# Kernel optimization log

Measured on AMD Instinct MI355X. Metric: run time of the kernel, lower is better.

Reference implementation:

```python
import jax, jax.numpy as jnp
import numpy as np

B, T, C = 2, 4096, 1024
H = 16            # n_head (== n_groups == n_kv_heads)
HD = C // H       # head_dim = 64
W = 256           # window_size
ROPE_BASE = 10000.0


def _rope(x):
    # x: (B, H, T, HD); rotate interleaved pairs with position along axis 2
    t = x.shape[2]
    inv_freq = 1.0 / (ROPE_BASE ** (jnp.arange(0, HD, 2, dtype=jnp.float32) / HD))  # (HD/2,)
    freqs = jnp.arange(t, dtype=jnp.float32)[:, None] * inv_freq[None, :]           # (T, HD/2)
    cos = jnp.cos(freqs)[None, None].astype(x.dtype)
    sin = jnp.sin(freqs)[None, None].astype(x.dtype)
    x1, x2 = x[..., 0::2], x[..., 1::2]
    o1 = x1 * cos - x2 * sin
    o2 = x1 * sin + x2 * cos
    return jnp.stack([o1, o2], axis=-1).reshape(x.shape)


def setup_inputs() -> dict:
    key = jax.random.key(0)
    ks = jax.random.split(key, 5)
    s = 1.0 / np.sqrt(C)
    return {
        "x": jax.random.normal(ks[0], (B, T, C), dtype=jnp.float32),
        "wq": jax.random.normal(ks[1], (C, C), dtype=jnp.float32) * s,
        "wk": jax.random.normal(ks[2], (C, C), dtype=jnp.float32) * s,
        "wv": jax.random.normal(ks[3], (C, C), dtype=jnp.float32) * s,
        "wo": jax.random.normal(ks[4], (C, C), dtype=jnp.float32) * s,
    }


def reference(x, wq, wk, wv, wo):
    # projections (Linear stores (out, in) -> x @ w.T)
    q = jnp.einsum('btc,oc->bto', x, wq).reshape(B, T, H, HD).transpose(0, 2, 1, 3)
    k = jnp.einsum('btc,oc->bto', x, wk).reshape(B, T, H, HD).transpose(0, 2, 1, 3)
    v = jnp.einsum('btc,oc->bto', x, wv).reshape(B, T, H, HD).transpose(0, 2, 1, 3)

    q = _rope(q)
    k = _rope(k)

    nW = T // W
    qw = q.reshape(B, H, nW, W, HD)
    kw = k.reshape(B, H, nW, W, HD)
    vw = v.reshape(B, H, nW, W, HD)

    scale = 1.0 / jnp.sqrt(jnp.asarray(HD, dtype=q.dtype))
    att = jnp.einsum('bhnqd,bhnkd->bhnqk', qw, kw) * scale   # per-window, no causal mask
    att = jax.nn.softmax(att, axis=-1)
    yw = jnp.einsum('bhnqk,bhnkd->bhnqd', att, vw)

    y = yw.reshape(B, H, T, HD).transpose(0, 2, 1, 3).reshape(B, T, C)
    return jnp.einsum('btc,oc->bto', y, wo)
```

## Files before the change

kernel.cpp:

```cpp
#include <hip/hip_runtime.h>
#include <math.h>

typedef float f32x4 __attribute__((ext_vector_type(4)));
typedef __bf16 bf16x8 __attribute__((ext_vector_type(8)));
typedef unsigned short u16x8 __attribute__((ext_vector_type(8)));
typedef unsigned short ushort_t;

#define MFMA16(a, b, c) __builtin_amdgcn_mfma_f32_16x16x32_bf16((a), (b), (c), 0, 0, 0)

static __device__ __forceinline__ ushort_t f2bf(float f) {
  union { float f; unsigned u; } v; v.f = f;
  unsigned u = v.u;
  return (ushort_t)((u + 0x7FFFu + ((u >> 16) & 1u)) >> 16);
}
static __device__ __forceinline__ float bf2f(ushort_t h) {
  union { unsigned u; float f; } v; v.u = ((unsigned)h) << 16;
  return v.f;
}
static __device__ __forceinline__ void gl_lds16(const void* g, void* lds_uniform) {
  __builtin_amdgcn_global_load_lds(
      (const __attribute__((address_space(1))) unsigned int*)g,
      (__attribute__((address_space(3))) unsigned int*)lds_uniform, 16, 0, 0);
}

__global__ void prep(const float* __restrict__ x,
                     const float* __restrict__ wq, const float* __restrict__ wk,
                     const float* __restrict__ wv, const float* __restrict__ wo,
                     ushort_t* __restrict__ Xb, ushort_t* __restrict__ Wqb,
                     ushort_t* __restrict__ Wkb, ushort_t* __restrict__ Wvb,
                     ushort_t* __restrict__ Wob, float2* __restrict__ cs) {
  const int bid = blockIdx.x;
  if (bid < 512) {
    int idx = bid * 256 + threadIdx.x;
    int pos = idx >> 5, i = idx & 31;
    double inv = exp2(-(double)i * 0.41524101186092029);
    double th = (double)pos * inv;
    double s, c;
    sincos(th, &s, &c);
    cs[idx] = make_float2((float)c, (float)s);
  } else {
    const float* src;
    ushort_t* dst;
    int i;
    if (bid < 8704) {
      src = x; dst = Xb;
      i = (bid - 512) * 256 + threadIdx.x;
    } else {
      const int wi = (bid - 8704) >> 10;
      src = (wi == 0) ? wq : (wi == 1) ? wk : (wi == 2) ? wv : wo;
      dst = (wi == 0) ? Wqb : (wi == 1) ? Wkb : (wi == 2) ? Wvb : Wob;
      i = ((bid - 8704) & 1023) * 256 + threadIdx.x;
    }
    f32x4 v = ((const f32x4*)src)[i];
    ushort4 o;
    o.x = f2bf(v.x); o.y = f2bf(v.y); o.z = f2bf(v.z); o.w = f2bf(v.w);
    ((ushort4*)dst)[i] = o;
  }
}

template <int OUTBF>
__global__ __launch_bounds__(256) void gemm_nt(
    const ushort_t* __restrict__ A,
    const ushort_t* __restrict__ W0, const ushort_t* __restrict__ W1, const ushort_t* __restrict__ W2,
    void* __restrict__ C0, void* __restrict__ C1, void* __restrict__ C2,
    int K, int N) {
  __shared__ __align__(16) ushort_t As[128 * 64];
  __shared__ __align__(16) ushort_t Bs[128 * 64];
  const int z = blockIdx.z;
  const ushort_t* W = (z == 0) ? W0 : (z == 1 ? W1 : W2);
  void* Cv = (z == 0) ? C0 : (z == 1 ? C1 : C2);

  const int t = threadIdx.x;
  const int lane = t & 63;
  const int l15 = lane & 15;
  const int quad = lane >> 4;
  const int wave = t >> 6;
  const int wm = wave & 1, wn = wave >> 1;
  const int bm = blockIdx.x, bn = blockIdx.y;

  const int srow = t >> 3;
  const int schunk = (t & 7) ^ (srow & 7);
  const ushort_t* Ag = A + (size_t)(bm * 128 + srow) * K + schunk * 8;
  const ushort_t* Wg = W + (size_t)(bn * 128 + srow) * K + schunk * 8;
  char* AsB = (char*)As + (t & 192) * 16;
  char* BsB = (char*)Bs + (t & 192) * 16;
  const size_t rK = (size_t)32 * K;

  const f32x4 zero4 = {0.f, 0.f, 0.f, 0.f};
  f32x4 acc[4][4];
#pragma unroll
  for (int i = 0; i < 4; ++i)
#pragma unroll
    for (int j = 0; j < 4; ++j) acc[i][j] = zero4;

  for (int kt = 0; kt < K; kt += 64) {
#pragma unroll
    for (int p = 0; p < 4; ++p) {
      gl_lds16(Ag + p * rK + kt, AsB + p * 4096);
      gl_lds16(Wg + p * rK + kt, BsB + p * 4096);
    }
    __syncthreads();
#pragma unroll
    for (int ks = 0; ks < 2; ++ks) {
      bf16x8 af[4], bfr[4];
#pragma unroll
      for (int i = 0; i < 4; ++i) {
        const int r = wm * 64 + i * 16 + l15;
        af[i] = *(const bf16x8*)&As[r * 64 + (((ks * 4 + quad) ^ (r & 7)) * 8)];
      }
#pragma unroll
      for (int j = 0; j < 4; ++j) {
        const int r = wn * 64 + j * 16 + l15;
        bfr[j] = *(const bf16x8*)&Bs[r * 64 + (((ks * 4 + quad) ^ (r & 7)) * 8)];
      }
#pragma unroll
      for (int i = 0; i < 4; ++i)
#pragma unroll
        for (int j = 0; j < 4; ++j) acc[i][j] = MFMA16(af[i], bfr[j], acc[i][j]);
    }
    __syncthreads();
  }

  const int rbase = bm * 128 + wm * 64 + quad * 4;
  const int cbase = bn * 128 + wn * 64 + l15;
#pragma unroll
  for (int i = 0; i < 4; ++i)
#pragma unroll
    for (int j = 0; j < 4; ++j)
#pragma unroll
      for (int r = 0; r < 4; ++r) {
        size_t idx = (size_t)(rbase + i * 16 + r) * N + (cbase + j * 16);
        if (OUTBF)
          ((ushort_t*)Cv)[idx] = f2bf(acc[i][j][r]);
        else
          ((float*)Cv)[idx] = acc[i][j][r];
      }
}

static __device__ __forceinline__ void rope8(const ushort_t* __restrict__ g,
                                             ushort_t* __restrict__ lds,
                                             const float2* __restrict__ cs4) {
  uint4 raw = *(const uint4*)g;
  unsigned rw[4] = {raw.x, raw.y, raw.z, raw.w};
  ushort_t o[8];
#pragma unroll
  for (int m = 0; m < 4; ++m) {
    float x1 = bf2f((ushort_t)(rw[m] & 0xffffu));
    float x2 = bf2f((ushort_t)(rw[m] >> 16));
    float2 sc = cs4[m];
    o[2 * m]     = f2bf(x1 * sc.x - x2 * sc.y);
    o[2 * m + 1] = f2bf(x1 * sc.y + x2 * sc.x);
  }
  uint4 w;
  w.x = (unsigned)o[0] | ((unsigned)o[1] << 16);
  w.y = (unsigned)o[2] | ((unsigned)o[3] << 16);
  w.z = (unsigned)o[4] | ((unsigned)o[5] << 16);
  w.w = (unsigned)o[6] | ((unsigned)o[7] << 16);
  *(uint4*)lds = w;
}

__global__ __launch_bounds__(256) void attn(
    const ushort_t* __restrict__ Qb, const ushort_t* __restrict__ Kb,
    const ushort_t* __restrict__ Vb, ushort_t* __restrict__ Yb,
    const float2* __restrict__ cs) {
  __shared__ __align__(16) ushort_t smem[21504];
  ushort_t* Ks = smem;
  ushort_t* Vt = smem;
  ushort_t* Pc = smem + 16896;

  const int t = threadIdx.x;
  const int lane = t & 63, wave = t >> 6;
  const int l15 = lane & 15, quad = lane >> 4;
  const int win = blockIdx.x >> 2, qq = blockIdx.x & 3;
  const int h = blockIdx.y, b = blockIdx.z;
  const int kBase = win * 256;
  const int qRow0 = kBase + qq * 64 + wave * 16;
  const size_t gbase = ((size_t)b * 4096) * 1024 + h * 64;

  const int sr = t >> 3;
  const int c0 = (t & 7) * 8;

#pragma unroll
  for (int p = 0; p < 8; ++p) {
    int r = p * 32 + sr;
    rope8(Kb + gbase + (size_t)(kBase + r) * 1024 + c0, Ks + r * 72 + c0,
          cs + (kBase + r) * 32 + (c0 >> 1));
  }
  __syncthreads();

  const f32x4 zero4 = {0.f, 0.f, 0.f, 0.f};
  f32x4 S[16];
#pragma unroll
  for (int j = 0; j < 16; ++j) S[j] = zero4;
#pragma unroll
  for (int ks = 0; ks < 2; ++ks) {
    union { u16x8 u; bf16x8 b; } aq;
    aq.u = *(const u16x8*)(Qb + gbase + (size_t)(qRow0 + l15) * 1024 + ks * 32 + quad * 8);
    const float2* csq = cs + (size_t)(qRow0 + l15) * 32 + ks * 16 + quad * 4;
#pragma unroll
    for (int m = 0; m < 4; ++m) {
      float x1 = bf2f(aq.u[2 * m]);
      float x2 = bf2f(aq.u[2 * m + 1]);
      float2 sc = csq[m];
      aq.u[2 * m]     = f2bf((x1 * sc.x - x2 * sc.y) * 0.125f);
      aq.u[2 * m + 1] = f2bf((x1 * sc.y + x2 * sc.x) * 0.125f);
    }
#pragma unroll
    for (int j = 0; j < 16; ++j) {
      bf16x8 bk = *(const bf16x8*)&Ks[(j * 16 + l15) * 72 + ks * 32 + quad * 8];
      S[j] = MFMA16(aq.b, bk, S[j]);
    }
  }

  float linv[4];
#pragma unroll
  for (int r = 0; r < 4; ++r) {
    float mx = S[0][r];
#pragma unroll
    for (int j = 1; j < 16; ++j) mx = fmaxf(mx, S[j][r]);
    mx = fmaxf(mx, __shfl_xor(mx, 1));
    mx = fmaxf(mx, __shfl_xor(mx, 2));
    mx = fmaxf(mx, __shfl_xor(mx, 4));
    mx = fmaxf(mx, __shfl_xor(mx, 8));
    float sum = 0.f;
#pragma unroll
    for (int j = 0; j < 16; ++j) {
      float e = __expf(S[j][r] - mx);
      S[j][r] = e;
      sum += e;
    }
    sum += __shfl_xor(sum, 1);
    sum += __shfl_xor(sum, 2);
    sum += __shfl_xor(sum, 4);
    sum += __shfl_xor(sum, 8);
    linv[r] = 1.0f / sum;
  }
  __syncthreads();

#pragma unroll
  for (int p = 0; p < 8; ++p) {
    int k = p * 32 + sr;
    uint4 raw = *(const uint4*)(Vb + gbase + (size_t)(kBase + k) * 1024 + c0);
    ushort_t vv[8];
    vv[0] = raw.x & 0xffffu; vv[1] = raw.x >> 16;
    vv[2] = raw.y & 0xffffu; vv[3] = raw.y >> 16;
    vv[4] = raw.z & 0xffffu; vv[5] = raw.z >> 16;
    vv[6] = raw.w & 0xffffu; vv[7] = raw.w >> 16;
#pragma unroll
    for (int e = 0; e < 8; ++e) {
      int ee = (e + (t & 7)) & 7;
      Vt[(c0 + ee) * 264 + k] = vv[ee];
    }
  }
  __syncthreads();

  const int qw = wave * 16;
  f32x4 O[4];
#pragma unroll
  for (int jd = 0; jd < 4; ++jd) O[jd] = zero4;

#pragma unroll
  for (int kc = 0; kc < 4; ++kc) {
#pragma unroll
    for (int jj = 0; jj < 4; ++jj) {
      int j = kc * 4 + jj;
#pragma unroll
      for (int r = 0; r < 4; ++r)
        Pc[(qw + quad * 4 + r) * 72 + jj * 16 + l15] = f2bf(S[j][r]);
    }
#pragma unroll
    for (int ks = 0; ks < 2; ++ks) {
      bf16x8 a = *(const bf16x8*)&Pc[(qw + l15) * 72 + ks * 32 + quad * 8];
#pragma unroll
      for (int jd = 0; jd < 4; ++jd) {
        bf16x8 bv = *(const bf16x8*)&Vt[(jd * 16 + l15) * 264 + kc * 64 + ks * 32 + quad * 8];
        O[jd] = MFMA16(a, bv, O[jd]);
      }
    }
  }

#pragma unroll
  for (int jd = 0; jd < 4; ++jd)
#pragma unroll
    for (int r = 0; r < 4; ++r) {
      int row = qRow0 + quad * 4 + r;
      Yb[gbase + (size_t)row * 1024 + jd * 16 + l15] = f2bf(O[jd][r] * linv[r]);
    }
}

extern "C" void kernel_launch(void* const* d_in, const int* in_sizes, int n_in,
                              void* d_out, int out_size, void* d_ws, size_t ws_size,
                              hipStream_t stream) {
  (void)in_sizes; (void)n_in; (void)out_size; (void)ws_size;
  const float* x  = (const float*)d_in[0];
  const float* wq = (const float*)d_in[1];
  const float* wk = (const float*)d_in[2];
  const float* wv = (const float*)d_in[3];
  const float* wo = (const float*)d_in[4];

  char* ws = (char*)d_ws;
  ushort_t* Xb  = (ushort_t*)(ws);
  ushort_t* Wqb = (ushort_t*)(ws + 16777216);
  ushort_t* Wkb = Wqb + 1048576;
  ushort_t* Wvb = Wkb + 1048576;
  ushort_t* Wob = Wvb + 1048576;
  ushort_t* Qb  = (ushort_t*)(ws + 25165824);
  ushort_t* Kb  = Qb + 8388608;
  ushort_t* Vb  = Kb + 8388608;
  ushort_t* Yb  = Vb + 8388608;
  float2*   cs  = (float2*)(ws + 92274688);

  prep<<<dim3(12800), dim3(256), 0, stream>>>(x, wq, wk, wv, wo,
                                              Xb, Wqb, Wkb, Wvb, Wob, cs);

  gemm_nt<1><<<dim3(64, 8, 3), dim3(256), 0, stream>>>(
      Xb, Wqb, Wkb, Wvb, (void*)Qb, (void*)Kb, (void*)Vb, 1024, 1024);

  attn<<<dim3(64, 16, 2), dim3(256), 0, stream>>>(Qb, Kb, Vb, Yb, cs);

  gemm_nt<0><<<dim3(64, 8, 1), dim3(256), 0, stream>>>(
      Yb, Wob, Wob, Wob, d_out, d_out, d_out, 1024, 1024);
}
```

Measured before the change: 248.1 us.

## Split RoPE into separate pass and restructure attention with transposed S and fp16 PV

Moves RoPE for Q and K out of the attention kernel into a standalone in-place pass, so attention can load K straight into swizzled LDS with async global_load_lds. It computes S transposed (K as the A operand) so each lane owns one query column, which removes the P round-trip through LDS and lets P feed an fp16 16x16x16 MFMA directly from registers. V is written as fp16 by the QKV GEMM, its loads are hoisted before the barrier, and the output is staged through LDS for coalesced 16-byte stores. This adds one extra kernel launch and a full read/write pass over Q and K, and changes V and P precision to fp16.

```diff
diff --git a/kernel.cpp b/kernel.cpp
--- a/kernel.cpp
+++ b/kernel.cpp
@@ -3,10 +3,11 @@
 
 typedef float f32x4 __attribute__((ext_vector_type(4)));
 typedef __bf16 bf16x8 __attribute__((ext_vector_type(8)));
-typedef unsigned short u16x8 __attribute__((ext_vector_type(8)));
+typedef _Float16 f16x4 __attribute__((ext_vector_type(4)));
 typedef unsigned short ushort_t;
 
 #define MFMA16(a, b, c) __builtin_amdgcn_mfma_f32_16x16x32_bf16((a), (b), (c), 0, 0, 0)
+#define MFMAPV(a, b, c) __builtin_amdgcn_mfma_f32_16x16x16f16((a), (b), (c), 0, 0, 0)
 
 static __device__ __forceinline__ ushort_t f2bf(float f) {
   union { float f; unsigned u; } v; v.f = f;
@@ -58,7 +59,7 @@
   }
 }
 
-template <int OUTBF>
+template <int MODE>
 __global__ __launch_bounds__(256) void gemm_nt(
     const ushort_t* __restrict__ A,
     const ushort_t* __restrict__ W0, const ushort_t* __restrict__ W1, const ushort_t* __restrict__ W2,
@@ -130,49 +131,67 @@
 #pragma unroll
       for (int r = 0; r < 4; ++r) {
         size_t idx = (size_t)(rbase + i * 16 + r) * N + (cbase + j * 16);
-        if (OUTBF)
+        if (MODE == 0) {
+          ((float*)Cv)[idx] = acc[i][j][r];
+        } else if (z == 2) {
+          union { _Float16 h; ushort_t u; } cv;
+          cv.h = (_Float16)acc[i][j][r];
+          ((ushort_t*)Cv)[idx] = cv.u;
+        } else {
           ((ushort_t*)Cv)[idx] = f2bf(acc[i][j][r]);
-        else
-          ((float*)Cv)[idx] = acc[i][j][r];
+        }
       }
 }
 
-static __device__ __forceinline__ void rope8(const ushort_t* __restrict__ g,
-                                             ushort_t* __restrict__ lds,
-                                             const float2* __restrict__ cs4) {
-  uint4 raw = *(const uint4*)g;
+static __device__ __forceinline__ uint4 rope_u4(uint4 raw, const float2* __restrict__ c4,
+                                                float scale) {
   unsigned rw[4] = {raw.x, raw.y, raw.z, raw.w};
   ushort_t o[8];
 #pragma unroll
   for (int m = 0; m < 4; ++m) {
     float x1 = bf2f((ushort_t)(rw[m] & 0xffffu));
     float x2 = bf2f((ushort_t)(rw[m] >> 16));
-    float2 sc = cs4[m];
-    o[2 * m]     = f2bf(x1 * sc.x - x2 * sc.y);
-    o[2 * m + 1] = f2bf(x1 * sc.y + x2 * sc.x);
+    float2 sc = c4[m];
+    o[2 * m]     = f2bf((x1 * sc.x - x2 * sc.y) * scale);
+    o[2 * m + 1] = f2bf((x1 * sc.y + x2 * sc.x) * scale);
   }
   uint4 w;
   w.x = (unsigned)o[0] | ((unsigned)o[1] << 16);
   w.y = (unsigned)o[2] | ((unsigned)o[3] << 16);
   w.z = (unsigned)o[4] | ((unsigned)o[5] << 16);
   w.w = (unsigned)o[6] | ((unsigned)o[7] << 16);
-  *(uint4*)lds = w;
+  return w;
+}
+
+__global__ void ropeqk(ushort_t* __restrict__ Qb, ushort_t* __restrict__ Kb,
+                       const float2* __restrict__ cs) {
+  const int idx0 = blockIdx.x * 256 + threadIdx.x;
+#pragma unroll
+  for (int g = 0; g < 2; ++g) {
+    const int idx = idx0 + g * 524288;
+    const int row = idx >> 7;
+    const int col8 = (idx & 127) << 3;
+    const float2* c4 = cs + (((size_t)(row & 4095)) << 5) + ((col8 & 63) >> 1);
+    uint4 q = ((const uint4*)Qb)[idx];
+    uint4 k = ((const uint4*)Kb)[idx];
+    ((uint4*)Qb)[idx] = rope_u4(q, c4, 0.125f);
+    ((uint4*)Kb)[idx] = rope_u4(k, c4, 1.0f);
+  }
 }
 
 __global__ __launch_bounds__(256) void attn(
     const ushort_t* __restrict__ Qb, const ushort_t* __restrict__ Kb,
-    const ushort_t* __restrict__ Vb, ushort_t* __restrict__ Yb,
-    const float2* __restrict__ cs) {
-  __shared__ __align__(16) ushort_t smem[21504];
+    const ushort_t* __restrict__ Vb, ushort_t* __restrict__ Yb) {
+  __shared__ __align__(16) ushort_t smem[16896];
   ushort_t* Ks = smem;
   ushort_t* Vt = smem;
-  ushort_t* Pc = smem + 16896;
 
   const int t = threadIdx.x;
   const int lane = t & 63, wave = t >> 6;
   const int l15 = lane & 15, quad = lane >> 4;
-  const int win = blockIdx.x >> 2, qq = blockIdx.x & 3;
-  const int h = blockIdx.y, b = blockIdx.z;
+  const int qq = blockIdx.x >> 9;
+  const int s = blockIdx.x & 511;
+  const int win = s & 15, h = (s >> 4) & 15, b = s >> 8;
   const int kBase = win * 256;
   const int qRow0 = kBase + qq * 64 + wave * 16;
   const size_t gbase = ((size_t)b * 4096) * 1024 + h * 64;
@@ -180,12 +199,17 @@
   const int sr = t >> 3;
   const int c0 = (t & 7) * 8;
 
-#pragma unroll
-  for (int p = 0; p < 8; ++p) {
-    int r = p * 32 + sr;
-    rope8(Kb + gbase + (size_t)(kBase + r) * 1024 + c0, Ks + r * 72 + c0,
-          cs + (kBase + r) * 32 + (c0 >> 1));
-  }
+  const int schunk = ((t & 7) ^ (sr & 7)) * 8;
+  const ushort_t* Kg = Kb + gbase + (size_t)(kBase + sr) * 1024 + schunk;
+  char* LdsB = (char*)smem + (t & 192) * 16;
+#pragma unroll
+  for (int p = 0; p < 8; ++p) gl_lds16(Kg + (size_t)p * 32 * 1024, LdsB + p * 4096);
+
+  bf16x8 qf[2];
+#pragma unroll
+  for (int ks = 0; ks < 2; ++ks)
+    qf[ks] = *(const bf16x8*)(Qb + gbase + (size_t)(qRow0 + l15) * 1024 + ks * 32 + quad * 8);
+
   __syncthreads();
 
   const f32x4 zero4 = {0.f, 0.f, 0.f, 0.f};
@@ -193,99 +217,84 @@
 #pragma unroll
   for (int j = 0; j < 16; ++j) S[j] = zero4;
 #pragma unroll
-  for (int ks = 0; ks < 2; ++ks) {
-    union { u16x8 u; bf16x8 b; } aq;
-    aq.u = *(const u16x8*)(Qb + gbase + (size_t)(qRow0 + l15) * 1024 + ks * 32 + quad * 8);
-    const float2* csq = cs + (size_t)(qRow0 + l15) * 32 + ks * 16 + quad * 4;
-#pragma unroll
-    for (int m = 0; m < 4; ++m) {
-      float x1 = bf2f(aq.u[2 * m]);
-      float x2 = bf2f(aq.u[2 * m + 1]);
-      float2 sc = csq[m];
-      aq.u[2 * m]     = f2bf((x1 * sc.x - x2 * sc.y) * 0.125f);
-      aq.u[2 * m + 1] = f2bf((x1 * sc.y + x2 * sc.x) * 0.125f);
-    }
+  for (int ks = 0; ks < 2; ++ks)
 #pragma unroll
     for (int j = 0; j < 16; ++j) {
-      bf16x8 bk = *(const bf16x8*)&Ks[(j * 16 + l15) * 72 + ks * 32 + quad * 8];
-      S[j] = MFMA16(aq.b, bk, S[j]);
-    }
-  }
-
-  float linv[4];
-#pragma unroll
-  for (int r = 0; r < 4; ++r) {
-    float mx = S[0][r];
-#pragma unroll
-    for (int j = 1; j < 16; ++j) mx = fmaxf(mx, S[j][r]);
-    mx = fmaxf(mx, __shfl_xor(mx, 1));
-    mx = fmaxf(mx, __shfl_xor(mx, 2));
-    mx = fmaxf(mx, __shfl_xor(mx, 4));
-    mx = fmaxf(mx, __shfl_xor(mx, 8));
-    float sum = 0.f;
-#pragma unroll
-    for (int j = 0; j < 16; ++j) {
-      float e = __expf(S[j][r] - mx);
-      S[j][r] = e;
-      sum += e;
-    }
-    sum += __shfl_xor(sum, 1);
-    sum += __shfl_xor(sum, 2);
-    sum += __shfl_xor(sum, 4);
-    sum += __shfl_xor(sum, 8);
-    linv[r] = 1.0f / sum;
-  }
+      bf16x8 kf = *(const bf16x8*)&Ks[(j * 16 + l15) * 64 + ((ks * 4 + quad) ^ (l15 & 7)) * 8];
+      S[j] = MFMA16(kf, qf[ks], S[j]);
+    }
+
+  float mx = S[0][0];
+#pragma unroll
+  for (int j = 0; j < 16; ++j)
+#pragma unroll
+    for (int e = 0; e < 4; ++e) mx = fmaxf(mx, S[j][e]);
+  mx = fmaxf(mx, __shfl_xor(mx, 16));
+  mx = fmaxf(mx, __shfl_xor(mx, 32));
+  float sum = 0.f;
+#pragma unroll
+  for (int j = 0; j < 16; ++j)
+#pragma unroll
+    for (int e = 0; e < 4; ++e) {
+      float e_ = __expf(S[j][e] - mx);
+      S[j][e] = e_;
+      sum += e_;
+    }
+  sum += __shfl_xor(sum, 16);
+  sum += __shfl_xor(sum, 32);
+  const float linv = 1.0f / sum;
+
+  f16x4 pf[16];
+#pragma unroll
+  for (int j = 0; j < 16; ++j) pf[j] = __builtin_convertvector(S[j], f16x4);
+
+  uint4 vraw[8];
+#pragma unroll
+  for (int p = 0; p < 8; ++p)
+    vraw[p] = *(const uint4*)(Vb + gbase + (size_t)(kBase + p * 32 + sr) * 1024 + c0);
+
   __syncthreads();
 
 #pragma unroll
   for (int p = 0; p < 8; ++p) {
-    int k = p * 32 + sr;
-    uint4 raw = *(const uint4*)(Vb + gbase + (size_t)(kBase + k) * 1024 + c0);
+    const int k = p * 32 + sr;
     ushort_t vv[8];
-    vv[0] = raw.x & 0xffffu; vv[1] = raw.x >> 16;
-    vv[2] = raw.y & 0xffffu; vv[3] = raw.y >> 16;
-    vv[4] = raw.z & 0xffffu; vv[5] = raw.z >> 16;
-    vv[6] = raw.w & 0xffffu; vv[7] = raw.w >> 16;
+    vv[0] = vraw[p].x & 0xffffu; vv[1] = vraw[p].x >> 16;
+    vv[2] = vraw[p].y & 0xffffu; vv[3] = vraw[p].y >> 16;
+    vv[4] = vraw[p].z & 0xffffu; vv[5] = vraw[p].z >> 16;
+    vv[6] = vraw[p].w & 0xffffu; vv[7] = vraw[p].w >> 16;
 #pragma unroll
     for (int e = 0; e < 8; ++e) {
-      int ee = (e + (t & 7)) & 7;
+      const int ee = (e + (t & 7)) & 7;
       Vt[(c0 + ee) * 264 + k] = vv[ee];
     }
   }
   __syncthreads();
 
-  const int qw = wave * 16;
   f32x4 O[4];
 #pragma unroll
   for (int jd = 0; jd < 4; ++jd) O[jd] = zero4;
-
-#pragma unroll
-  for (int kc = 0; kc < 4; ++kc) {
-#pragma unroll
-    for (int jj = 0; jj < 4; ++jj) {
-      int j = kc * 4 + jj;
-#pragma unroll
-      for (int r = 0; r < 4; ++r)
-        Pc[(qw + quad * 4 + r) * 72 + jj * 16 + l15] = f2bf(S[j][r]);
-    }
-#pragma unroll
-    for (int ks = 0; ks < 2; ++ks) {
-      bf16x8 a = *(const bf16x8*)&Pc[(qw + l15) * 72 + ks * 32 + quad * 8];
-#pragma unroll
-      for (int jd = 0; jd < 4; ++jd) {
-        bf16x8 bv = *(const bf16x8*)&Vt[(jd * 16 + l15) * 264 + kc * 64 + ks * 32 + quad * 8];
-        O[jd] = MFMA16(a, bv, O[jd]);
-      }
-    }
-  }
-
+#pragma unroll
+  for (int j = 0; j < 16; ++j)
+#pragma unroll
+    for (int jd = 0; jd < 4; ++jd) {
+      f16x4 vf = *(const f16x4*)&Vt[(jd * 16 + l15) * 264 + j * 16 + quad * 4];
+      O[jd] = MFMAPV(vf, pf[j], O[jd]);
+    }
+
+  __syncthreads();
+
+  ushort_t* tile = smem + wave * 1152;
 #pragma unroll
   for (int jd = 0; jd < 4; ++jd)
 #pragma unroll
-    for (int r = 0; r < 4; ++r) {
-      int row = qRow0 + quad * 4 + r;
-      Yb[gbase + (size_t)row * 1024 + jd * 16 + l15] = f2bf(O[jd][r] * linv[r]);
-    }
+    for (int r = 0; r < 4; ++r)
+      tile[l15 * 72 + jd * 16 + quad * 4 + r] = f2bf(O[jd][r] * linv);
+#pragma unroll
+  for (int g = 0; g < 2; ++g) {
+    uint4 w = *(const uint4*)&tile[l15 * 72 + quad * 16 + g * 8];
+    *(uint4*)(Yb + gbase + (size_t)(qRow0 + l15) * 1024 + quad * 16 + g * 8) = w;
+  }
 }
 
 extern "C" void kernel_launch(void* const* d_in, const int* in_sizes, int n_in,
@@ -316,7 +325,9 @@
   gemm_nt<1><<<dim3(64, 8, 3), dim3(256), 0, stream>>>(
       Xb, Wqb, Wkb, Wvb, (void*)Qb, (void*)Kb, (void*)Vb, 1024, 1024);
 
-  attn<<<dim3(64, 16, 2), dim3(256), 0, stream>>>(Qb, Kb, Vb, Yb, cs);
+  ropeqk<<<dim3(2048), dim3(256), 0, stream>>>(Qb, Kb, cs);
+
+  attn<<<dim3(2048), dim3(256), 0, stream>>>(Qb, Kb, Vb, Yb);
 
   gemm_nt<0><<<dim3(64, 8, 1), dim3(256), 0, stream>>>(
       Yb, Wob, Wob, Wob, d_out, d_out, d_out, 1024, 1024);
```

Measured after the change: 231.5 us. 6.7% less time.
